# Optimization experiments

Measured on AMD Instinct MI355X. Metric: run time of the kernel, lower is better.

## Reference

```python
import jax, jax.numpy as jnp
import numpy as np
from jax.scipy.linalg import solve_triangular

B, M, S, NBPS = 32768, 16, 8, 4
NUM_ITER = 2
EPS = 1e-4

def _pam_gray(b):
    if len(b) > 1:
        return (1 - 2 * b[0]) * (2 ** len(b[1:]) - _pam_gray(b[1:]))
    return 1 - 2 * b[0]

def _qam(nbps):
    n = 2 ** nbps
    pts = np.zeros(n, np.complex64)
    for i in range(n):
        b = np.array([int(c) for c in np.binary_repr(i, nbps)])
        pts[i] = _pam_gray(b[0::2]) + 1j * _pam_gray(b[1::2])
    pts = pts / np.sqrt(np.mean(np.abs(pts) ** 2))
    labels = ((np.arange(n)[:, None] >> np.arange(nbps - 1, -1, -1)) & 1).astype(np.float32)
    return pts.astype(np.complex64), labels

_PTS_NP, _LAB_NP = _qam(NBPS)
PTS = jnp.asarray(_PTS_NP)                                   # [P] complex64, unit-energy Gray QAM16
PTS_E = jnp.asarray((np.abs(_PTS_NP) ** 2).astype(np.float32))  # [P]
LAB = jnp.asarray(_LAB_NP)                                   # [P, K] bit labels (MSB first)
ASGN = 2.0 * LAB - 1.0                                       # [P, K], +1 where bit==1

def _symbol_logits(llr):
    # LLRs2SymbolLogits: llr=[...,S,K] (llr = log p(b=1)/p(b=0)) -> per-point log-prior [...,S,P]
    return jnp.sum(jax.nn.log_sigmoid(ASGN * llr[..., None, :]), axis=-1)

def _moments(logits):
    # SymbolLogits2Moments: softmax over points -> mean / variance of soft symbols
    p = jax.nn.softmax(logits, axis=-1)                       # [..., S, P]
    mean = jnp.einsum('...p,p->...', p.astype(jnp.complex64), PTS)
    e2 = jnp.einsum('...p,p->...', p, PTS_E)
    var = e2 - (mean.real ** 2 + mean.imag ** 2)
    return mean, var

def _demap(x_hat, llr_a, no_eff):
    # maxlog DemapperWithPrior, LLR = log p(b=1)/p(b=0)
    diff = x_hat[..., None] - PTS                             # [..., S, P]
    d2 = diff.real ** 2 + diff.imag ** 2
    exps = -d2 / no_eff[..., None] + _symbol_logits(llr_a)    # [..., S, P]
    e = exps[..., None]                                       # [..., S, P, 1]
    neg = jnp.float32(-1e30)
    l1 = jnp.max(jnp.where(LAB == 1.0, e, neg), axis=-2)      # [..., S, K]
    l0 = jnp.max(jnp.where(LAB == 0.0, e, neg), axis=-2)
    return l1 - l0

def _forward(y_re, y_im, h_re, h_im, prior, s_re, s_im):
    y = jax.lax.complex(y_re, y_im)                           # [B, M]
    h = jax.lax.complex(h_re, h_im)                           # [B, M, S]
    s = jax.lax.complex(s_re, s_im)                           # [B, M, M] Hermitian PSD
    # whiten_channel: s = L L^H, y <- L^-1 y, h <- L^-1 h
    L = jnp.linalg.cholesky(s)
    y = solve_triangular(L, y[..., None], lower=True)[..., 0]
    h = solve_triangular(L, h, lower=True)
    y_mf = jnp.einsum('bms,bm->bs', jnp.conj(h), y)[..., None]   # [B, S, 1] matched filter
    g = jnp.einsum('bmi,bmj->bij', jnp.conj(h), h)               # [B, S, S] Gram matrix
    # real-valued channel representation [[Re,-Im],[Im,Re]]
    hr = jnp.concatenate([
        jnp.concatenate([h.real, -h.imag], axis=-1),
        jnp.concatenate([h.imag, h.real], axis=-1)], axis=-2)    # [B, 2M, 2S]
    gr = jnp.einsum('bmi,bmj->bij', hr, hr)                      # [B, 2S, 2S]
    eye2s = jnp.eye(2 * S, dtype=jnp.float32)
    llr_d = prior
    llr_a = jnp.zeros_like(prior)
    for _ in range(NUM_ITER):
        llr_a = llr_d
        x_hat, var_x = _moments(_symbol_logits(llr_a))           # [B, S]
        # parallel interference cancellation in matched-filter domain
        y_mf_pic = (y_mf + g * x_hat[..., None, :]
                    - jnp.einsum('bij,bj->bi', g, x_hat)[..., None])  # [B, S, S]
        var2 = jnp.concatenate([var_x, var_x], axis=-1)          # [B, 2S]
        a = gr * var2[..., None, :] + eye2s                      # [B, 2S, 2S]
        a_inv = jnp.linalg.inv(a)
        mu = jnp.sum(a_inv * jnp.swapaxes(gr, -1, -2), axis=-1)  # diag(a_inv @ gr), [B, 2S]
        ypt = jnp.swapaxes(y_mf_pic, -1, -2)                     # [B, S, S] (stream-major)
        ypt_r = jnp.concatenate([ypt.real, ypt.imag], axis=-1)   # [B, S, 2S]
        ypt_r = jnp.concatenate([ypt_r, ypt_r], axis=-2)         # [B, 2S, 2S]
        z = jnp.sum(a_inv * ypt_r, axis=-1) / mu                 # [B, 2S] unbiased estimates
        zr, zi = jnp.split(z, 2, axis=-1)
        x_hat = jax.lax.complex(zr, zi)                          # [B, S]
        rho = mu / jnp.maximum(1.0 - var2 * mu, EPS)             # post-equalization SINR
        rho = jnp.split(rho, 2, axis=-1)[0]                      # [B, S]
        no_eff = 1.0 / rho
        llr_d = _demap(x_hat, llr_a, no_eff)
    return llr_d - llr_a  # extrinsic LLRs [B, S, K]

def setup_inputs() -> dict:
    key = jax.random.key(0)
    k = jax.random.split(key, 7)
    y_re = jax.random.normal(k[0], (B, M), jnp.float32)
    y_im = jax.random.normal(k[1], (B, M), jnp.float32)
    h_re = jax.random.normal(k[2], (B, M, S), jnp.float32) / np.float32(np.sqrt(2.0))
    h_im = jax.random.normal(k[3], (B, M, S), jnp.float32) / np.float32(np.sqrt(2.0))
    prior = 0.5 * jax.random.normal(k[4], (B, S, NBPS), jnp.float32)
    a = jax.lax.complex(jax.random.normal(k[5], (B, M, M), jnp.float32),
                        jax.random.normal(k[6], (B, M, M), jnp.float32)) / np.float32(np.sqrt(2.0 * M))
    s = jnp.einsum('bij,bkj->bik', a, jnp.conj(a)) + 0.5 * jnp.eye(M, dtype=jnp.complex64)
    return {"y_re": y_re, "y_im": y_im, "h_re": h_re, "h_im": h_im,
            "prior": prior, "s_re": s.real, "s_im": s.imag}

def reference(y_re, y_im, h_re, h_im, prior, s_re, s_im):
    return _forward(y_re, y_im, h_re, h_im, prior, s_re, s_im)
```

## Files before the change

kernel.cpp:

```cpp
#include <hip/hip_runtime.h>


#define EPS_F 1e-4f
#define INV_SQRT10 0.31622776601683794f
#define WSYNC() __builtin_amdgcn_wave_barrier()

typedef float v2f __attribute__((ext_vector_type(2)));

__device__ __forceinline__ float rcpf(float x) { return __builtin_amdgcn_rcpf(x); }
__device__ __forceinline__ float rsqf(float x) { return __builtin_amdgcn_rsqf(x); }
__device__ __forceinline__ float rdlane(float v, int l) {
    return __uint_as_float(__builtin_amdgcn_readlane(__float_as_uint(v), l));
}
template<int OFF>
__device__ __forceinline__ float swzf(float v) {
    return __uint_as_float(__builtin_amdgcn_ds_swizzle(__float_as_uint(v), OFF));
}
#define SWX1 0x041F
#define SWX2 0x081F
#define SWX4 0x101F

__device__ __forceinline__ float pt_re(int p) {
    return (1.0f - 2.0f * (float)((p >> 3) & 1)) * (1.0f + 2.0f * (float)((p >> 1) & 1)) * INV_SQRT10;
}
__device__ __forceinline__ float pt_im(int p) {
    return (1.0f - 2.0f * (float)((p >> 2) & 1)) * (1.0f + 2.0f * (float)(p & 1)) * INV_SQRT10;
}

__global__ __launch_bounds__(128, 4)
void mmse_pic_kernel(const float* __restrict__ y_re, const float* __restrict__ y_im,
                     const float* __restrict__ h_re, const float* __restrict__ h_im,
                     const float* __restrict__ prior,
                     const float* __restrict__ s_re, const float* __restrict__ s_im,
                     float* __restrict__ out)
{
    const int lane = threadIdx.x & 63;
    const int w    = threadIdx.x >> 6;
    const int b    = blockIdx.x * 2 + w;
    const size_t bs = (size_t)b;

    __shared__ v2f   Sc[2][16][28];
    __shared__ v2f   xc_[2][8];
    __shared__ v2f   ymc_[2][8];
    __shared__ float vx_[2][8], ne_[2][8];
    __shared__ float lsig[2][64];
    __shared__ float logit_[2][8][20];
    __shared__ float llrD_[2][8][4];

    {
        const float4* pr4 = (const float4*)(s_re + bs * 256);
        const float4* pi4 = (const float4*)(s_im + bs * 256);
        float4 vr = pr4[lane], vi = pi4[lane];
        int r = lane >> 2, c0 = (lane & 3) << 2;
        Sc[w][r][c0+0] = (v2f){vr.x, vi.x};
        Sc[w][r][c0+1] = (v2f){vr.y, vi.y};
        Sc[w][r][c0+2] = (v2f){vr.z, vi.z};
        Sc[w][r][c0+3] = (v2f){vr.w, vi.w};
        if (lane < 32) {
            const float4* hr4 = (const float4*)(h_re + bs * 128);
            const float4* hi4 = (const float4*)(h_im + bs * 128);
            float4 hr = hr4[lane], hi = hi4[lane];
            int row = lane >> 1, col = 16 + ((lane & 1) << 2);
            Sc[w][row][col+0] = (v2f){hr.x, hi.x};
            Sc[w][row][col+1] = (v2f){hr.y, hi.y};
            Sc[w][row][col+2] = (v2f){hr.z, hi.z};
            Sc[w][row][col+3] = (v2f){hr.w, hi.w};
        }
        if (lane < 16) Sc[w][lane][24] = (v2f){y_re[bs*16+lane], y_im[bs*16+lane]};
        if (lane < 32) ((float*)llrD_[w])[lane] = prior[bs*32 + lane];
    }
    WSYNC();

    {
        const int j0 = lane & 15;
        const int r4 = lane >> 4;
        #pragma unroll
        for (int k = 0; k < 15; ++k) {
            float invd = rcpf(Sc[w][k][k].x);
            int j1 = k + 1 + j0, j2 = j1 + 16;
            v2f rk0 = (v2f){0.f, 0.f}, rk1 = (v2f){0.f, 0.f};
            if (j1 < 25) rk0 = Sc[w][k][j1];
            const bool blk2 = (k < 8);
            if (blk2 && j2 < 25) rk1 = Sc[w][k][j2];
            v2f rk0A = (v2f){-rk0.y, rk0.x};
            v2f rk1A = (v2f){-rk1.y, rk1.x};
            const int pmin = (k + 1) >> 2;
            #pragma unroll
            for (int p = 0; p < 4; ++p) {
                if (p < pmin) continue;
                int i = (p << 2) + r4;
                v2f aik = Sc[w][i][k];
                v2f mv = aik * invd;
                if (i <= k) mv = (v2f){0.f, 0.f};
                if (j1 < 25) {
                    v2f a = Sc[w][i][j1];
                    a -= mv.x * rk0;
                    a -= mv.y * rk0A;
                    Sc[w][i][j1] = a;
                }
                if (blk2 && j2 < 25) {
                    v2f a = Sc[w][i][j2];
                    a -= mv.x * rk1;
                    a -= mv.y * rk1A;
                    Sc[w][i][j2] = a;
                }
            }
            WSYNC();
        }
    }
    {
        int r2 = lane >> 2, c = lane & 3;
        float irs = rsqf(Sc[w][r2][r2].x);
        Sc[w][r2][16 + c] = Sc[w][r2][16 + c] * irs;
        Sc[w][r2][20 + c] = Sc[w][r2][20 + c] * irs;
        if (c == 0) Sc[w][r2][24] = Sc[w][r2][24] * irs;
    }
    WSYNC();

    const int s = lane >> 3, u = lane & 7;
    v2f G1 = (v2f){0.f, 0.f}, G2 = (v2f){0.f, 0.f};
    v2f Y1 = (v2f){0.f, 0.f}, Y2 = (v2f){0.f, 0.f};
    #pragma unroll
    for (int m = 0; m < 16; ++m) {
        v2f a  = Sc[w][m][16 + s];
        v2f x  = Sc[w][m][16 + u];
        v2f xy = Sc[w][m][24];
        G1 += a.x * x;   G2 += a.y * x;
        Y1 += a.x * xy;  Y2 += a.y * xy;
    }
    const float g_re = G1.x + G2.y;
    const float g_im = G1.y - G2.x;
    if (u == 0) ymc_[w][s] = (v2f){Y1.x + Y2.y, Y1.y - Y2.x};
    WSYNC();

    const float pr = pt_re(u), pi2 = pt_im(u), pe = pr*pr + pi2*pi2;
    float llr_a_reg = 0.f;

    for (int it = 0; it < 2; ++it) {
        {
            int ts = lane >> 3, tk = (lane >> 1) & 3, sg = lane & 1;
            float v = llrD_[w][ts][tk];
            float x = sg ? v : -v;
            lsig[w][lane] = fminf(x, 0.f) - __logf(1.0f + __expf(-fabsf(x)));
        }
        if (lane < 32) llr_a_reg = ((float*)llrD_[w])[lane];
        WSYNC();
        int base = s << 3;
        float lc = lsig[w][base | 2 | ((u >> 2) & 1)]
                 + lsig[w][base | 4 | ((u >> 1) & 1)]
                 + lsig[w][base | 6 | (u & 1)];
        float l0 = lc + lsig[w][base];
        float l1 = lc + lsig[w][base | 1];
        {
            float mx = fmaxf(l0, l1);
            mx = fmaxf(mx, swzf<SWX1>(mx));
            mx = fmaxf(mx, swzf<SWX2>(mx));
            mx = fmaxf(mx, swzf<SWX4>(mx));
            float w0 = __expf(l0 - mx), w1 = __expf(l1 - mx);
            float a = w0 + w1, dw = w0 - w1;
            float se = a, mr = dw * pr, mi = a * pi2, e2 = a * pe;
            se += swzf<SWX1>(se); mr += swzf<SWX1>(mr); mi += swzf<SWX1>(mi); e2 += swzf<SWX1>(e2);
            se += swzf<SWX2>(se); mr += swzf<SWX2>(mr); mi += swzf<SWX2>(mi); e2 += swzf<SWX2>(e2);
            se += swzf<SWX4>(se); mr += swzf<SWX4>(mr); mi += swzf<SWX4>(mi); e2 += swzf<SWX4>(e2);
            if (u == 0) {
                float inv = rcpf(se);
                float mxr = mr*inv, mxi = mi*inv;
                xc_[w][s] = (v2f){mxr, mxi};
                vx_[w][s] = e2*inv - (mxr*mxr + mxi*mxi);
            }
        }
        WSYNC();
        v2f xj = xc_[w][u];
        float vj = vx_[w][u];
        float tr = g_re*xj.x - g_im*xj.y;
        float ti = g_re*xj.y + g_im*xj.x;
        tr += swzf<SWX1>(tr); ti += swzf<SWX1>(ti);
        tr += swzf<SWX2>(tr); ti += swzf<SWX2>(ti);
        tr += swzf<SWX4>(tr); ti += swzf<SWX4>(ti);
        v2f ym = ymc_[w][s];
        float br_ = ym.x - tr, bi_ = ym.y - ti;
        float Ar = g_re*vj + ((s == u) ? 1.f : 0.f);
        float Ai = g_im*vj;
        float Cr = g_re, Ci = g_im;
        #define GJ_STEP(K) { \
            float pvr = rdlane(Ar, (K)*9), pvi = rdlane(Ai, (K)*9); \
            int rowsrc = ((K)<<3)|u; \
            float rAr = __shfl(Ar, rowsrc), rAi = __shfl(Ai, rowsrc); \
            float rCr = __shfl(Cr, rowsrc), rCi = __shfl(Ci, rowsrc); \
            float rbr = __shfl(br_, rowsrc), rbi = __shfl(bi_, rowsrc); \
            float cAr = swzf<(((K)<<5)|0x18)>(Ar), cAi = swzf<(((K)<<5)|0x18)>(Ai); \
            float id2 = rcpf(pvr*pvr + pvi*pvi); \
            float ipr2 = pvr*id2, ipi2 = -pvi*id2; \
            float mr2 = cAr*ipr2 - cAi*ipi2; \
            float mi2 = cAr*ipi2 + cAi*ipr2; \
            if (s == (K)) { mr2 = 0.f; mi2 = 0.f; } \
            Ar  -= mr2*rAr - mi2*rAi;  Ai  -= mr2*rAi + mi2*rAr; \
            Cr  -= mr2*rCr - mi2*rCi;  Ci  -= mr2*rCi + mi2*rCr; \
            br_ -= mr2*rbr - mi2*rbi;  bi_ -= mr2*rbi + mi2*rbr; }
        GJ_STEP(0) GJ_STEP(1) GJ_STEP(2) GJ_STEP(3)
        GJ_STEP(4) GJ_STEP(5) GJ_STEP(6) GJ_STEP(7)
        #undef GJ_STEP
        if (s == u) {
            float id3 = rcpf(Ar*Ar + Ai*Ai);
            float ipr3 = Ar*id3, ipi3 = -Ai*id3;
            float wr = br_*ipr3 - bi_*ipi3;
            float wi = br_*ipi3 + bi_*ipr3;
            float ccr = Cr*ipr3 - Ci*ipi3;
            float cci = Cr*ipi3 + Ci*ipr3;
            float mu = ccr;
            float im = rcpf(mu);
            float zr = (wr + ccr*xj.x - cci*xj.y) * im;
            float zi = (wi + ccr*xj.y + cci*xj.x) * im;
            xc_[w][s] = (v2f){zr, zi};
            ne_[w][s] = fmaxf(1.f - vx_[w][s]*mu, EPS_F) * im;
        }
        WSYNC();
        {
            v2f xh = xc_[w][s];
            float idn = rcpf(ne_[w][s]);
            float dr0 = xh.x - pr, dr1 = xh.x + pr, di = xh.y - pi2;
            logit_[w][s][u]     = l0 - (dr0*dr0 + di*di) * idn;
            logit_[w][s][u + 8] = l1 - (dr1*dr1 + di*di) * idn;
        }
        WSYNC();
        {
            int s2 = lane >> 3, kb = (lane >> 1) & 3, half = lane & 1;
            int bitpos = 3 - kb;
            float m = -1e30f;
            #pragma unroll
            for (int q = 0; q < 8; ++q) {
                int low  = q & ((1 << bitpos) - 1);
                int high = (q >> bitpos) << (bitpos + 1);
                int p = high | (half << bitpos) | low;
                m = fmaxf(m, logit_[w][s2][p]);
            }
            float other = swzf<SWX1>(m);
            if (half == 1) llrD_[w][s2][kb] = m - other;
        }
        WSYNC();
    }

    if (lane < 32) out[bs*32 + lane] = ((float*)llrD_[w])[lane] - llr_a_reg;
}

extern "C" void kernel_launch(void* const* d_in, const int* in_sizes, int n_in,
                              void* d_out, int out_size, void* d_ws, size_t ws_size,
                              hipStream_t stream) {
    const float* y_re  = (const float*)d_in[0];
    const float* y_im  = (const float*)d_in[1];
    const float* h_re  = (const float*)d_in[2];
    const float* h_im  = (const float*)d_in[3];
    const float* prior = (const float*)d_in[4];
    const float* s_re  = (const float*)d_in[5];
    const float* s_im  = (const float*)d_in[6];
    float* out = (float*)d_out;

    const int B = in_sizes[0] / 16;
    mmse_pic_kernel<<<dim3(B / 2), dim3(128), 0, stream>>>(
        y_re, y_im, h_re, h_im, prior, s_re, s_im, out);
}
```

Measured before the change: 241.2 us.

## Use DPP cross-lane ops, vectorized LDS elimination, and register-based max-log demap

Replaces ds_swizzle xor reductions with DPP row moves, which avoid the LDS pipeline. The Gaussian elimination on the augmented matrix now processes two complex columns per lane with float4 LDS loads and stores, with clamped column indices. The max-log demapper no longer stages logits through shared memory. It computes per-bit maxima with DPP/swizzle butterflies in registers, which removes one barrier and an 8-iteration LDS loop. The risks are redundant overlapping writes from the clamped lanes and correctness of the new bit-mapping butterflies.

New measurement: 242.8 us. Within noise of the previous version (+0.6%).

```diff
diff --git a/kernel.cpp b/kernel.cpp
--- a/kernel.cpp
+++ b/kernel.cpp
@@ -16,9 +16,14 @@
 __device__ __forceinline__ float swzf(float v) {
     return __uint_as_float(__builtin_amdgcn_ds_swizzle(__float_as_uint(v), OFF));
 }
-#define SWX1 0x041F
-#define SWX2 0x081F
-#define SWX4 0x101F
+template<int CTRL>
+__device__ __forceinline__ float dppf(float v) {
+    return __int_as_float(__builtin_amdgcn_mov_dpp(__float_as_int(v), CTRL, 0xF, 0xF, true));
+}
+#define DPP_X1 0xB1
+#define DPP_X2 0x4E
+#define DPP_M8 0x141
+#define SWX4   0x101F
 
 __device__ __forceinline__ float pt_re(int p) {
     return (1.0f - 2.0f * (float)((p >> 3) & 1)) * (1.0f + 2.0f * (float)((p >> 1) & 1)) * INV_SQRT10;
@@ -39,12 +44,11 @@
     const int b    = blockIdx.x * 2 + w;
     const size_t bs = (size_t)b;
 
-    __shared__ v2f   Sc[2][16][28];
+    __shared__ __align__(16) v2f Sc[2][16][28];
     __shared__ v2f   xc_[2][8];
     __shared__ v2f   ymc_[2][8];
     __shared__ float vx_[2][8], ne_[2][8];
     __shared__ float lsig[2][64];
-    __shared__ float logit_[2][8][20];
     __shared__ float llrD_[2][8][4];
 
     {
@@ -72,38 +76,31 @@
     WSYNC();
 
     {
-        const int j0 = lane & 15;
         const int r4 = lane >> 4;
+        int jpr = lane & 15;
+        const int jp = (jpr > 13) ? 13 : jpr;
         #pragma unroll
         for (int k = 0; k < 15; ++k) {
             float invd = rcpf(Sc[w][k][k].x);
-            int j1 = k + 1 + j0, j2 = j1 + 16;
-            v2f rk0 = (v2f){0.f, 0.f}, rk1 = (v2f){0.f, 0.f};
-            if (j1 < 25) rk0 = Sc[w][k][j1];
-            const bool blk2 = (k < 8);
-            if (blk2 && j2 < 25) rk1 = Sc[w][k][j2];
-            v2f rk0A = (v2f){-rk0.y, rk0.x};
-            v2f rk1A = (v2f){-rk1.y, rk1.x};
-            const int pmin = (k + 1) >> 2;
+            float4 rk = *(const float4*)&Sc[w][k][2*jp];
+            const int p0 = k >> 2;
             #pragma unroll
             for (int p = 0; p < 4; ++p) {
-                if (p < pmin) continue;
+                if (p < p0) continue;
                 int i = (p << 2) + r4;
                 v2f aik = Sc[w][i][k];
-                v2f mv = aik * invd;
-                if (i <= k) mv = (v2f){0.f, 0.f};
-                if (j1 < 25) {
-                    v2f a = Sc[w][i][j1];
-                    a -= mv.x * rk0;
-                    a -= mv.y * rk0A;
-                    Sc[w][i][j1] = a;
+                float mr = aik.x * invd, mi = aik.y * invd;
+                if (p == p0) {
+                    bool dead = (i <= k);
+                    mr = dead ? 0.f : mr;
+                    mi = dead ? 0.f : mi;
                 }
-                if (blk2 && j2 < 25) {
-                    v2f a = Sc[w][i][j2];
-                    a -= mv.x * rk1;
-                    a -= mv.y * rk1A;
-                    Sc[w][i][j2] = a;
-                }
+                float4 a = *(float4*)&Sc[w][i][2*jp];
+                a.x -= mr*rk.x - mi*rk.y;
+                a.y -= mr*rk.y + mi*rk.x;
+                a.z -= mr*rk.z - mi*rk.w;
+                a.w -= mr*rk.w + mi*rk.z;
+                *(float4*)&Sc[w][i][2*jp] = a;
             }
             WSYNC();
         }
@@ -111,26 +108,30 @@
     {
         int r2 = lane >> 2, c = lane & 3;
         float irs = rsqf(Sc[w][r2][r2].x);
-        Sc[w][r2][16 + c] = Sc[w][r2][16 + c] * irs;
-        Sc[w][r2][20 + c] = Sc[w][r2][20 + c] * irs;
-        if (c == 0) Sc[w][r2][24] = Sc[w][r2][24] * irs;
+        v2f v0 = Sc[w][r2][16 + c];
+        Sc[w][r2][16 + c] = (v2f){v0.x*irs, v0.y*irs};
+        v2f v1 = Sc[w][r2][20 + c];
+        Sc[w][r2][20 + c] = (v2f){v1.x*irs, v1.y*irs};
+        if (c == 0) {
+            v2f v2 = Sc[w][r2][24];
+            Sc[w][r2][24] = (v2f){v2.x*irs, v2.y*irs};
+        }
     }
     WSYNC();
 
     const int s = lane >> 3, u = lane & 7;
-    v2f G1 = (v2f){0.f, 0.f}, G2 = (v2f){0.f, 0.f};
-    v2f Y1 = (v2f){0.f, 0.f}, Y2 = (v2f){0.f, 0.f};
+    float g_re = 0.f, g_im = 0.f, ym_r = 0.f, ym_i = 0.f;
     #pragma unroll
     for (int m = 0; m < 16; ++m) {
         v2f a  = Sc[w][m][16 + s];
         v2f x  = Sc[w][m][16 + u];
         v2f xy = Sc[w][m][24];
-        G1 += a.x * x;   G2 += a.y * x;
-        Y1 += a.x * xy;  Y2 += a.y * xy;
-    }
-    const float g_re = G1.x + G2.y;
-    const float g_im = G1.y - G2.x;
-    if (u == 0) ymc_[w][s] = (v2f){Y1.x + Y2.y, Y1.y - Y2.x};
+        g_re += a.x*x.x + a.y*x.y;
+        g_im += a.x*x.y - a.y*x.x;
+        ym_r += a.x*xy.x + a.y*xy.y;
+        ym_i += a.x*xy.y - a.y*xy.x;
+    }
+    if (u == 0) ymc_[w][s] = (v2f){ym_r, ym_i};
     WSYNC();
 
     const float pr = pt_re(u), pi2 = pt_im(u), pe = pr*pr + pi2*pi2;
@@ -153,15 +154,15 @@
         float l1 = lc + lsig[w][base | 1];
         {
             float mx = fmaxf(l0, l1);
-            mx = fmaxf(mx, swzf<SWX1>(mx));
-            mx = fmaxf(mx, swzf<SWX2>(mx));
-            mx = fmaxf(mx, swzf<SWX4>(mx));
+            mx = fmaxf(mx, dppf<DPP_X1>(mx));
+            mx = fmaxf(mx, dppf<DPP_X2>(mx));
+            mx = fmaxf(mx, dppf<DPP_M8>(mx));
             float w0 = __expf(l0 - mx), w1 = __expf(l1 - mx);
             float a = w0 + w1, dw = w0 - w1;
             float se = a, mr = dw * pr, mi = a * pi2, e2 = a * pe;
-            se += swzf<SWX1>(se); mr += swzf<SWX1>(mr); mi += swzf<SWX1>(mi); e2 += swzf<SWX1>(e2);
-            se += swzf<SWX2>(se); mr += swzf<SWX2>(mr); mi += swzf<SWX2>(mi); e2 += swzf<SWX2>(e2);
-            se += swzf<SWX4>(se); mr += swzf<SWX4>(mr); mi += swzf<SWX4>(mi); e2 += swzf<SWX4>(e2);
+            se += dppf<DPP_X1>(se); mr += dppf<DPP_X1>(mr); mi += dppf<DPP_X1>(mi); e2 += dppf<DPP_X1>(e2);
+            se += dppf<DPP_X2>(se); mr += dppf<DPP_X2>(mr); mi += dppf<DPP_X2>(mi); e2 += dppf<DPP_X2>(e2);
+            se += dppf<DPP_M8>(se); mr += dppf<DPP_M8>(mr); mi += dppf<DPP_M8>(mi); e2 += dppf<DPP_M8>(e2);
             if (u == 0) {
                 float inv = rcpf(se);
                 float mxr = mr*inv, mxi = mi*inv;
@@ -174,9 +175,9 @@
         float vj = vx_[w][u];
         float tr = g_re*xj.x - g_im*xj.y;
         float ti = g_re*xj.y + g_im*xj.x;
-        tr += swzf<SWX1>(tr); ti += swzf<SWX1>(ti);
-        tr += swzf<SWX2>(tr); ti += swzf<SWX2>(ti);
-        tr += swzf<SWX4>(tr); ti += swzf<SWX4>(ti);
+        tr += dppf<DPP_X1>(tr); ti += dppf<DPP_X1>(ti);
+        tr += dppf<DPP_X2>(tr); ti += dppf<DPP_X2>(ti);
+        tr += dppf<DPP_M8>(tr); ti += dppf<DPP_M8>(ti);
         v2f ym = ymc_[w][s];
         float br_ = ym.x - tr, bi_ = ym.y - ti;
         float Ar = g_re*vj + ((s == u) ? 1.f : 0.f);
@@ -215,27 +216,31 @@
             ne_[w][s] = fmaxf(1.f - vx_[w][s]*mu, EPS_F) * im;
         }
         WSYNC();
+        v2f xh = xc_[w][s];
+        float idn = rcpf(ne_[w][s]);
+        float dr0 = xh.x - pr, dr1 = xh.x + pr, di = xh.y - pi2;
+        float e0 = l0 - (dr0*dr0 + di*di) * idn;
+        float e1 = l1 - (dr1*dr1 + di*di) * idn;
         {
-            v2f xh = xc_[w][s];
-            float idn = rcpf(ne_[w][s]);
-            float dr0 = xh.x - pr, dr1 = xh.x + pr, di = xh.y - pi2;
-            logit_[w][s][u]     = l0 - (dr0*dr0 + di*di) * idn;
-            logit_[w][s][u + 8] = l1 - (dr1*dr1 + di*di) * idn;
-        }
-        WSYNC();
-        {
-            int s2 = lane >> 3, kb = (lane >> 1) & 3, half = lane & 1;
-            int bitpos = 3 - kb;
-            float m = -1e30f;
-            #pragma unroll
-            for (int q = 0; q < 8; ++q) {
-                int low  = q & ((1 << bitpos) - 1);
-                int high = (q >> bitpos) << (bitpos + 1);
-                int p = high | (half << bitpos) | low;
-                m = fmaxf(m, logit_[w][s2][p]);
+            float e = fmaxf(e0, e1);
+            float h0 = e0;
+            h0 = fmaxf(h0, dppf<DPP_X1>(h0)); h0 = fmaxf(h0, dppf<DPP_X2>(h0)); h0 = fmaxf(h0, dppf<DPP_M8>(h0));
+            float h1 = e1;
+            h1 = fmaxf(h1, dppf<DPP_X1>(h1)); h1 = fmaxf(h1, dppf<DPP_X2>(h1)); h1 = fmaxf(h1, dppf<DPP_M8>(h1));
+            float L0 = h1 - h0;
+            float s12 = fmaxf(e, dppf<DPP_X1>(e)); s12 = fmaxf(s12, dppf<DPP_X2>(s12));
+            float s12p = swzf<SWX4>(s12);
+            float L1 = (u & 4) ? (s12 - s12p) : (s12p - s12);
+            float s14 = fmaxf(e, dppf<DPP_X1>(e)); s14 = fmaxf(s14, swzf<SWX4>(s14));
+            float s14p = dppf<DPP_X2>(s14);
+            float L2 = (u & 2) ? (s14 - s14p) : (s14p - s14);
+            float s24 = fmaxf(e, dppf<DPP_X2>(e)); s24 = fmaxf(s24, swzf<SWX4>(s24));
+            float s24p = dppf<DPP_X1>(s24);
+            float L3 = (u & 1) ? (s24 - s24p) : (s24p - s24);
+            if (u < 4) {
+                float Lsel = (u == 0) ? L0 : (u == 1) ? L1 : (u == 2) ? L2 : L3;
+                llrD_[w][s][u] = Lsel;
             }
-            float other = swzf<SWX1>(m);
-            if (half == 1) llrD_[w][s2][kb] = m - other;
         }
         WSYNC();
     }
```
